# Performance work log

Measured on AMD Instinct MI355X. Metric: run time of the kernel, lower is better.

## Reference

```python
import jax, jax.numpy as jnp
import numpy as np

DIM = 768
HEADS = 12
HEAD_DIM = DIM // HEADS
SCALE = HEAD_DIM ** -0.5


def setup_inputs() -> dict:
    key = jax.random.key(0)
    ks = jax.random.split(key, 6)
    B, N = 4, 2048
    x = jax.random.normal(ks[0], (B, N, DIM), dtype=jnp.float32)
    s = DIM ** -0.5
    Wq = jax.random.normal(ks[1], (DIM, DIM), dtype=jnp.float32) * s
    Wk = jax.random.normal(ks[2], (DIM, DIM), dtype=jnp.float32) * s
    Wv = jax.random.normal(ks[3], (DIM, DIM), dtype=jnp.float32) * s
    Wp = jax.random.normal(ks[4], (DIM, DIM), dtype=jnp.float32) * s
    bp = jnp.zeros((DIM,), dtype=jnp.float32)
    return {"x": x, "Wq": Wq, "Wk": Wk, "Wv": Wv, "Wp": Wp, "bp": bp}


def reference(x, Wq, Wk, Wv, Wp, bp):
    B, N, C = x.shape
    # separate Q/K/V linears (no bias, qkv_bias=False); torch Linear: x @ W.T
    q = (x @ Wq.T).reshape(B, N, HEADS, HEAD_DIM).transpose(0, 2, 1, 3)
    k = (x @ Wk.T).reshape(B, N, HEADS, HEAD_DIM).transpose(0, 2, 1, 3)
    v = (x @ Wv.T).reshape(B, N, HEADS, HEAD_DIM).transpose(0, 2, 1, 3)
    # explicit full [B,H,N,N] attention matrix, as in the source
    attn = jnp.einsum("bhqd,bhkd->bhqk", q, k) * SCALE
    attn = jax.nn.softmax(attn, axis=-1)
    out = jnp.einsum("bhqk,bhkd->bhqd", attn, v)
    out = out.transpose(0, 2, 1, 3).reshape(B, N, C)
    return out @ Wp.T + bp
```

## Files before the change

### kernel.cpp

```cpp
#include <hip/hip_runtime.h>
#include <cstdint>

#define DIM   768
#define HEADS 12
#define HDIM  64
#define BATCH 4
#define SEQ   2048
#define MROWS (BATCH*SEQ)
#define PSTR  72

typedef __bf16 bf16;
typedef __bf16 bf16x4_t __attribute__((ext_vector_type(4)));
typedef __bf16 bf16x8_t __attribute__((ext_vector_type(8)));
typedef float  f32x4_t  __attribute__((ext_vector_type(4)));

__global__ void cast_bf16_kernel(const float* __restrict__ src, bf16* __restrict__ dst, int n4) {
    int i = blockIdx.x * blockDim.x + threadIdx.x;
    if (i >= n4) return;
    const float4 v = reinterpret_cast<const float4*>(src)[i];
    bf16x4_t o;
    o[0] = (bf16)v.x; o[1] = (bf16)v.y; o[2] = (bf16)v.z; o[3] = (bf16)v.w;
    reinterpret_cast<bf16x4_t*>(dst)[i] = o;
}

__device__ __forceinline__ void gload_lds16(const bf16* g, bf16* l) {
    __builtin_amdgcn_global_load_lds((const __attribute__((address_space(1))) void*)g,
                                     (__attribute__((address_space(3))) void*)l, 16, 0, 0);
}

__global__ __launch_bounds__(256, 2) void qkv_gemm(
        const bf16* __restrict__ X,
        const bf16* __restrict__ Wq, const bf16* __restrict__ Wk, const bf16* __restrict__ Wv,
        bf16* __restrict__ Q, bf16* __restrict__ Kd, bf16* __restrict__ Vt)
{
    __shared__ bf16 As[128*32];
    __shared__ bf16 Bs[128*32];
    const int tid  = threadIdx.x;
    const int z    = blockIdx.z;
    const bf16* W  = (z == 0) ? Wq : (z == 1 ? Wk : Wv);
    const int n0   = blockIdx.x * 128;
    const int m0   = blockIdx.y * 128;
    const int lane = tid & 63;
    const int w    = tid >> 6;
    const int wm   = (w & 1) * 64, wn = (w >> 1) * 64;
    const int lr   = lane & 15, quad = lane >> 4;

    f32x4_t acc[4][4] = {};

    for (int kk = 0; kk < DIM; kk += 32) {
        #pragma unroll
        for (int i = 0; i < 2; ++i) {
            int c = tid + i * 256;
            int row = c >> 2, ko = (c & 3) * 8;
            gload_lds16(X + (size_t)(m0 + row) * DIM + kk + ko, &As[row * 32 + ko]);
            gload_lds16(W + (size_t)(n0 + row) * DIM + kk + ko, &Bs[row * 32 + ko]);
        }
        __syncthreads();
        bf16x8_t af[4], bfr[4];
        #pragma unroll
        for (int i = 0; i < 4; ++i)
            af[i] = *reinterpret_cast<const bf16x8_t*>(&As[(wm + i * 16 + lr) * 32 + quad * 8]);
        #pragma unroll
        for (int j = 0; j < 4; ++j)
            bfr[j] = *reinterpret_cast<const bf16x8_t*>(&Bs[(wn + j * 16 + lr) * 32 + quad * 8]);
        #pragma unroll
        for (int i = 0; i < 4; ++i)
            #pragma unroll
            for (int j = 0; j < 4; ++j)
                acc[i][j] = __builtin_amdgcn_mfma_f32_16x16x32_bf16(af[i], bfr[j], acc[i][j], 0, 0, 0);
        __syncthreads();
    }

    #pragma unroll
    for (int i = 0; i < 4; ++i) {
        int mbase = m0 + wm + i * 16 + quad * 4;
        #pragma unroll
        for (int j = 0; j < 4; ++j) {
            int n = n0 + wn + j * 16 + lr;
            int h = n >> 6, d = n & 63;
            #pragma unroll
            for (int r = 0; r < 4; ++r) {
                int m = mbase + r;
                int b = m >> 11, row = m & 2047;
                bf16 v = (bf16)acc[i][j][r];
                if (z < 2) {
                    bf16* dst = (z == 0) ? Q : Kd;
                    dst[(((size_t)b * HEADS + h) * SEQ + row) * HDIM + d] = v;
                } else {
                    Vt[(((size_t)b * HEADS + h) * HDIM + d) * SEQ + row] = v;
                }
            }
        }
    }
}

__global__ __launch_bounds__(256, 2) void out_gemm(
        const bf16* __restrict__ A,
        const bf16* __restrict__ W,
        const float* __restrict__ bias,
        float* __restrict__ out)
{
    __shared__ bf16 As[128*32];
    __shared__ bf16 Bs[128*32];
    const int tid  = threadIdx.x;
    const int n0   = blockIdx.x * 128;
    const int m0   = blockIdx.y * 128;
    const int lane = tid & 63;
    const int w    = tid >> 6;
    const int wm   = (w & 1) * 64, wn = (w >> 1) * 64;
    const int lr   = lane & 15, quad = lane >> 4;

    f32x4_t acc[4][4] = {};

    for (int kk = 0; kk < DIM; kk += 32) {
        #pragma unroll
        for (int i = 0; i < 2; ++i) {
            int c = tid + i * 256;
            int row = c >> 2, ko = (c & 3) * 8;
            gload_lds16(A + (size_t)(m0 + row) * DIM + kk + ko, &As[row * 32 + ko]);
            gload_lds16(W + (size_t)(n0 + row) * DIM + kk + ko, &Bs[row * 32 + ko]);
        }
        __syncthreads();
        bf16x8_t af[4], bfr[4];
        #pragma unroll
        for (int i = 0; i < 4; ++i)
            af[i] = *reinterpret_cast<const bf16x8_t*>(&As[(wm + i * 16 + lr) * 32 + quad * 8]);
        #pragma unroll
        for (int j = 0; j < 4; ++j)
            bfr[j] = *reinterpret_cast<const bf16x8_t*>(&Bs[(wn + j * 16 + lr) * 32 + quad * 8]);
        #pragma unroll
        for (int i = 0; i < 4; ++i)
            #pragma unroll
            for (int j = 0; j < 4; ++j)
                acc[i][j] = __builtin_amdgcn_mfma_f32_16x16x32_bf16(af[i], bfr[j], acc[i][j], 0, 0, 0);
        __syncthreads();
    }

    #pragma unroll
    for (int i = 0; i < 4; ++i) {
        int mbase = m0 + wm + i * 16 + quad * 4;
        #pragma unroll
        for (int j = 0; j < 4; ++j) {
            int n = n0 + wn + j * 16 + lr;
            float bv = bias[n];
            #pragma unroll
            for (int r = 0; r < 4; ++r) {
                int m = mbase + r;
                out[(size_t)m * DIM + n] = acc[i][j][r] + bv;
            }
        }
    }
}

__global__ __launch_bounds__(256, 2) void attn_kernel(
        const bf16* __restrict__ Q, const bf16* __restrict__ Kd,
        const bf16* __restrict__ Vt, bf16* __restrict__ Ab)
{
    __shared__ __align__(16) bf16 KV[2][2][64*64];
    __shared__ __align__(16) bf16 Ps[4][32*PSTR];

    const int tid  = threadIdx.x;
    const int bh   = blockIdx.y;
    const int b    = bh / HEADS, h = bh % HEADS;
    const int q0   = blockIdx.x * 128;
    const int lane = tid & 63, w = tid >> 6;
    const int lr   = lane & 15, quad = lane >> 4;
    const int wq   = w * 32;

    const size_t qkbase = (size_t)bh * SEQ * HDIM;
    const size_t vbase  = (size_t)bh * HDIM * SEQ;

    {
        bf16* Qst = &KV[1][0][0];
        #pragma unroll
        for (int i = 0; i < 4; ++i) {
            int c = tid + i * 256;
            int row = c >> 3, ch = c & 7;
            int gch = ch ^ (row & 7);
            gload_lds16(Q + qkbase + (size_t)(q0 + row) * HDIM + gch * 8, &Qst[row * 64 + ch * 8]);
        }
    }
    auto stageKV = [&](int it, int buf) {
        #pragma unroll
        for (int i = 0; i < 2; ++i) {
            int c = tid + i * 256;
            int row = c >> 3, ch = c & 7;
            int gch = ch ^ (row & 7);
            gload_lds16(Kd + qkbase + (size_t)(it * 64 + row) * HDIM + gch * 8,
                        &KV[buf][0][row * 64 + ch * 8]);
            gload_lds16(Vt + vbase + (size_t)row * SEQ + it * 64 + gch * 8,
                        &KV[buf][1][row * 64 + ch * 8]);
        }
    };
    stageKV(0, 0);
    __syncthreads();

    bf16x8_t qf[2][2];
    {
        const bf16* Qst = &KV[1][0][0];
        #pragma unroll
        for (int q16 = 0; q16 < 2; ++q16) {
            int row = wq + q16 * 16 + lr;
            #pragma unroll
            for (int ks = 0; ks < 2; ++ks) {
                int ch = (ks * 4 + quad) ^ (row & 7);
                qf[q16][ks] = *reinterpret_cast<const bf16x8_t*>(&Qst[row * 64 + ch * 8]);
            }
        }
    }
    __syncthreads();

    f32x4_t oacc[2][4] = {};
    float rs[2] = {0.f, 0.f};

    for (int it = 0; it < SEQ / 64; ++it) {
        const int buf = it & 1;
        if (it + 1 < SEQ / 64) stageKV(it + 1, buf ^ 1);

        const bf16* Ks = &KV[buf][0][0];
        const bf16* Vs = &KV[buf][1][0];

        f32x4_t sacc[4][2] = {};
        #pragma unroll
        for (int ks = 0; ks < 2; ++ks) {
            bf16x8_t af[4];
            #pragma unroll
            for (int kt = 0; kt < 4; ++kt) {
                int row = kt * 16 + lr;
                int ch = (ks * 4 + quad) ^ (row & 7);
                af[kt] = *reinterpret_cast<const bf16x8_t*>(&Ks[row * 64 + ch * 8]);
            }
            #pragma unroll
            for (int kt = 0; kt < 4; ++kt)
                #pragma unroll
                for (int q16 = 0; q16 < 2; ++q16)
                    sacc[kt][q16] = __builtin_amdgcn_mfma_f32_16x16x32_bf16(
                        af[kt], qf[q16][ks], sacc[kt][q16], 0, 0, 0);
        }

        #pragma unroll
        for (int kt = 0; kt < 4; ++kt) {
            #pragma unroll
            for (int q16 = 0; q16 < 2; ++q16) {
                bf16x4_t pk;
                float s0 = 0.f;
                #pragma unroll
                for (int r = 0; r < 4; ++r) {
                    float p = __expf(sacc[kt][q16][r] * 0.125f);
                    s0 += p;
                    pk[r] = (bf16)p;
                }
                rs[q16] += s0;
                *reinterpret_cast<bf16x4_t*>(&Ps[w][(q16 * 16 + lr) * PSTR + kt * 16 + quad * 4]) = pk;
            }
        }

        #pragma unroll
        for (int ks = 0; ks < 2; ++ks) {
            bf16x8_t ap[2], bv[4];
            #pragma unroll
            for (int q16 = 0; q16 < 2; ++q16)
                ap[q16] = *reinterpret_cast<const bf16x8_t*>(
                    &Ps[w][(q16 * 16 + lr) * PSTR + ks * 32 + quad * 8]);
            #pragma unroll
            for (int dt = 0; dt < 4; ++dt) {
                int row = dt * 16 + lr;
                int ch = (ks * 4 + quad) ^ (row & 7);
                bv[dt] = *reinterpret_cast<const bf16x8_t*>(&Vs[row * 64 + ch * 8]);
            }
            #pragma unroll
            for (int q16 = 0; q16 < 2; ++q16)
                #pragma unroll
                for (int dt = 0; dt < 4; ++dt)
                    oacc[q16][dt] = __builtin_amdgcn_mfma_f32_16x16x32_bf16(
                        ap[q16], bv[dt], oacc[q16][dt], 0, 0, 0);
        }
        __syncthreads();
    }

    #pragma unroll
    for (int q16 = 0; q16 < 2; ++q16) {
        rs[q16] += __shfl_xor(rs[q16], 16);
        rs[q16] += __shfl_xor(rs[q16], 32);
    }

    #pragma unroll
    for (int q16 = 0; q16 < 2; ++q16) {
        float inv[4];
        #pragma unroll
        for (int r = 0; r < 4; ++r)
            inv[r] = 1.0f / __shfl(rs[q16], quad * 4 + r);
        #pragma unroll
        for (int dt = 0; dt < 4; ++dt) {
            #pragma unroll
            for (int r = 0; r < 4; ++r) {
                int q = q0 + wq + q16 * 16 + quad * 4 + r;
                Ab[((size_t)b * SEQ + q) * DIM + h * HDIM + dt * 16 + lr] =
                    (bf16)(oacc[q16][dt][r] * inv[r]);
            }
        }
    }
}

extern "C" void kernel_launch(void* const* d_in, const int* in_sizes, int n_in,
                              void* d_out, int out_size, void* d_ws, size_t ws_size,
                              hipStream_t stream) {
    (void)in_sizes; (void)n_in; (void)out_size; (void)ws_size;
    const float* x  = (const float*)d_in[0];
    const float* Wq = (const float*)d_in[1];
    const float* Wk = (const float*)d_in[2];
    const float* Wv = (const float*)d_in[3];
    const float* Wp = (const float*)d_in[4];
    const float* bp = (const float*)d_in[5];
    float* out = (float*)d_out;

    char* ws = (char*)d_ws;
    size_t off = 0;
    auto alloc = [&](size_t bytes) {
        void* p = ws + off;
        off += (bytes + 255) & ~(size_t)255;
        return p;
    };
    const size_t big = (size_t)MROWS * DIM * sizeof(bf16);
    const size_t wsz = (size_t)DIM * DIM * sizeof(bf16);
    bf16* Xb  = (bf16*)alloc(big);
    bf16* Qb  = (bf16*)alloc(big);
    bf16* Kb  = (bf16*)alloc(big);
    bf16* Vtb = (bf16*)alloc(big);
    bf16* Wqb = (bf16*)alloc(wsz);
    bf16* Wkb = (bf16*)alloc(wsz);
    bf16* Wvb = (bf16*)alloc(wsz);
    bf16* Wpb = (bf16*)alloc(wsz);
    bf16* Ab  = Xb;

    const int x4 = MROWS * DIM / 4;
    cast_bf16_kernel<<<(x4 + 255) / 256, 256, 0, stream>>>(x, Xb, x4);
    const int w4 = DIM * DIM / 4;
    cast_bf16_kernel<<<(w4 + 255) / 256, 256, 0, stream>>>(Wq, Wqb, w4);
    cast_bf16_kernel<<<(w4 + 255) / 256, 256, 0, stream>>>(Wk, Wkb, w4);
    cast_bf16_kernel<<<(w4 + 255) / 256, 256, 0, stream>>>(Wv, Wvb, w4);
    cast_bf16_kernel<<<(w4 + 255) / 256, 256, 0, stream>>>(Wp, Wpb, w4);

    qkv_gemm<<<dim3(DIM / 128, MROWS / 128, 3), 256, 0, stream>>>(Xb, Wqb, Wkb, Wvb, Qb, Kb, Vtb);

    attn_kernel<<<dim3(SEQ / 128, BATCH * HEADS), 256, 0, stream>>>(Qb, Kb, Vtb, Ab);

    out_gemm<<<dim3(DIM / 128, MROWS / 128), 256, 0, stream>>>(Ab, Wpb, bp, out);
}
```

Before: 257.3 us.

## Keep softmax probabilities in registers for PV MFMA, merge weight casts

The attention kernel drops its shared-memory P staging buffer. It feeds the exponentiated scores straight from the S accumulator layout into 16x16x16 bf16 MFMAs, loading V fragments to match that layout. It also switches to exp2 with a pre-folded log2e scale, raises the launch-bounds occupancy target to 4, and fuses the four weight-cast launches into one. This cuts LDS traffic and launch overhead, at the cost of using twice as many smaller MFMA instructions and putting more pressure on registers.

```diff
diff --git a/kernel.cpp b/kernel.cpp
--- a/kernel.cpp
+++ b/kernel.cpp
@@ -7,16 +7,44 @@
 #define BATCH 4
 #define SEQ   2048
 #define MROWS (BATCH*SEQ)
-#define PSTR  72
 
 typedef __bf16 bf16;
 typedef __bf16 bf16x4_t __attribute__((ext_vector_type(4)));
 typedef __bf16 bf16x8_t __attribute__((ext_vector_type(8)));
 typedef float  f32x4_t  __attribute__((ext_vector_type(4)));
+typedef short  short4_t __attribute__((ext_vector_type(4)));
+
+__device__ __forceinline__ f32x4_t mfma16x16x16bf16(bf16x4_t a, bf16x4_t b, f32x4_t c) {
+#if __has_builtin(__builtin_amdgcn_mfma_f32_16x16x16_bf16)
+    return __builtin_amdgcn_mfma_f32_16x16x16_bf16(a, b, c, 0, 0, 0);
+#elif __has_builtin(__builtin_amdgcn_mfma_f32_16x16x16bf16_1k)
+    union U { bf16x4_t h; short4_t s; };
+    U ua, ub; ua.h = a; ub.h = b;
+    return __builtin_amdgcn_mfma_f32_16x16x16bf16_1k(ua.s, ub.s, c, 0, 0, 0);
+#else
+    asm("v_mfma_f32_16x16x16_bf16 %0, %1, %2, %0" : "+v"(c) : "v"(a), "v"(b));
+    return c;
+#endif
+}
 
 __global__ void cast_bf16_kernel(const float* __restrict__ src, bf16* __restrict__ dst, int n4) {
     int i = blockIdx.x * blockDim.x + threadIdx.x;
     if (i >= n4) return;
+    const float4 v = reinterpret_cast<const float4*>(src)[i];
+    bf16x4_t o;
+    o[0] = (bf16)v.x; o[1] = (bf16)v.y; o[2] = (bf16)v.z; o[3] = (bf16)v.w;
+    reinterpret_cast<bf16x4_t*>(dst)[i] = o;
+}
+
+__global__ void cast_w4_kernel(const float* __restrict__ s0, const float* __restrict__ s1,
+                               const float* __restrict__ s2, const float* __restrict__ s3,
+                               bf16* __restrict__ d0, bf16* __restrict__ d1,
+                               bf16* __restrict__ d2, bf16* __restrict__ d3, int n4) {
+    int i = blockIdx.x * blockDim.x + threadIdx.x;
+    if (i >= n4) return;
+    int y = blockIdx.y;
+    const float* src = (y == 0) ? s0 : (y == 1) ? s1 : (y == 2) ? s2 : s3;
+    bf16* dst        = (y == 0) ? d0 : (y == 1) ? d1 : (y == 2) ? d2 : d3;
     const float4 v = reinterpret_cast<const float4*>(src)[i];
     bf16x4_t o;
     o[0] = (bf16)v.x; o[1] = (bf16)v.y; o[2] = (bf16)v.z; o[3] = (bf16)v.w;
@@ -152,12 +180,11 @@
     }
 }
 
-__global__ __launch_bounds__(256, 2) void attn_kernel(
+__global__ __launch_bounds__(256, 4) void attn_kernel(
         const bf16* __restrict__ Q, const bf16* __restrict__ Kd,
         const bf16* __restrict__ Vt, bf16* __restrict__ Ab)
 {
     __shared__ __align__(16) bf16 KV[2][2][64*64];
-    __shared__ __align__(16) bf16 Ps[4][32*PSTR];
 
     const int tid  = threadIdx.x;
     const int bh   = blockIdx.y;
@@ -212,6 +239,7 @@
 
     f32x4_t oacc[2][4] = {};
     float rs[2] = {0.f, 0.f};
+    const float c_scale = 0.18033688011112042f;
 
     for (int it = 0; it < SEQ / 64; ++it) {
         const int buf = it & 1;
@@ -240,40 +268,28 @@
 
         #pragma unroll
         for (int kt = 0; kt < 4; ++kt) {
+            bf16x4_t bv[4];
+            #pragma unroll
+            for (int dt = 0; dt < 4; ++dt) {
+                int row = dt * 16 + lr;
+                int ch = (2 * kt + (quad >> 1)) ^ (row & 7);
+                bv[dt] = *reinterpret_cast<const bf16x4_t*>(&Vs[row * 64 + ch * 8 + (quad & 1) * 4]);
+            }
             #pragma unroll
             for (int q16 = 0; q16 < 2; ++q16) {
                 bf16x4_t pk;
                 float s0 = 0.f;
                 #pragma unroll
                 for (int r = 0; r < 4; ++r) {
-                    float p = __expf(sacc[kt][q16][r] * 0.125f);
+                    float p = __builtin_amdgcn_exp2f(sacc[kt][q16][r] * c_scale);
                     s0 += p;
                     pk[r] = (bf16)p;
                 }
                 rs[q16] += s0;
-                *reinterpret_cast<bf16x4_t*>(&Ps[w][(q16 * 16 + lr) * PSTR + kt * 16 + quad * 4]) = pk;
-            }
-        }
-
-        #pragma unroll
-        for (int ks = 0; ks < 2; ++ks) {
-            bf16x8_t ap[2], bv[4];
-            #pragma unroll
-            for (int q16 = 0; q16 < 2; ++q16)
-                ap[q16] = *reinterpret_cast<const bf16x8_t*>(
-                    &Ps[w][(q16 * 16 + lr) * PSTR + ks * 32 + quad * 8]);
-            #pragma unroll
-            for (int dt = 0; dt < 4; ++dt) {
-                int row = dt * 16 + lr;
-                int ch = (ks * 4 + quad) ^ (row & 7);
-                bv[dt] = *reinterpret_cast<const bf16x8_t*>(&Vs[row * 64 + ch * 8]);
-            }
-            #pragma unroll
-            for (int q16 = 0; q16 < 2; ++q16)
                 #pragma unroll
                 for (int dt = 0; dt < 4; ++dt)
-                    oacc[q16][dt] = __builtin_amdgcn_mfma_f32_16x16x32_bf16(
-                        ap[q16], bv[dt], oacc[q16][dt], 0, 0, 0);
+                    oacc[q16][dt] = mfma16x16x16bf16(pk, bv[dt], oacc[q16][dt]);
+            }
         }
         __syncthreads();
     }
@@ -336,10 +352,8 @@
     const int x4 = MROWS * DIM / 4;
     cast_bf16_kernel<<<(x4 + 255) / 256, 256, 0, stream>>>(x, Xb, x4);
     const int w4 = DIM * DIM / 4;
-    cast_bf16_kernel<<<(w4 + 255) / 256, 256, 0, stream>>>(Wq, Wqb, w4);
-    cast_bf16_kernel<<<(w4 + 255) / 256, 256, 0, stream>>>(Wk, Wkb, w4);
-    cast_bf16_kernel<<<(w4 + 255) / 256, 256, 0, stream>>>(Wv, Wvb, w4);
-    cast_bf16_kernel<<<(w4 + 255) / 256, 256, 0, stream>>>(Wp, Wpb, w4);
+    cast_w4_kernel<<<dim3((w4 + 255) / 256, 4), 256, 0, stream>>>(
+        Wq, Wk, Wv, Wp, Wqb, Wkb, Wvb, Wpb, w4);
 
     qkv_gemm<<<dim3(DIM / 128, MROWS / 128, 3), 256, 0, stream>>>(Xb, Wqb, Wkb, Wvb, Qb, Kb, Vtb);
 
```

Result: no change. 252.3 us (-1.9%).
